# Optimization experiments

Measured on AMD Instinct MI355X. Metric: run time of the kernel, lower is better.

The kernel has to match this reference:

```python
import jax, jax.numpy as jnp
import numpy as np

N_NODES = 100000


def gcn_conv(x, src, dst, W, b, n):
    # PyG GCNConv: h = x @ W; add self-loops; sym-normalize; scatter-add; + bias
    h = x @ W                                        # [N, out]
    loop = jnp.arange(n, dtype=src.dtype)
    src2 = jnp.concatenate([src, loop])              # [E+N]
    dst2 = jnp.concatenate([dst, loop])
    deg = jax.ops.segment_sum(jnp.ones_like(dst2, dtype=h.dtype), dst2, num_segments=n)
    dis = jnp.where(deg > 0, jax.lax.rsqrt(deg), 0.0)
    norm = dis[src2] * dis[dst2]                     # [E+N]
    msg = h[src2] * norm[:, None]                    # gather + scale
    out = jax.ops.segment_sum(msg, dst2, num_segments=n)  # scatter-add
    return out + b


def setup_inputs() -> dict:
    key = jax.random.key(0)
    ks = jax.random.split(key, 8)
    F_in, H = 128, 64
    E = 1200000
    x = jax.random.normal(ks[0], (N_NODES, F_in), dtype=jnp.float32)
    edge_index = jax.random.randint(ks[1], (2, E), 0, N_NODES, dtype=jnp.int64)
    s = 1.0 / np.sqrt(F_in)
    W1 = jax.random.normal(ks[2], (F_in, H), dtype=jnp.float32) * s
    b1 = jnp.zeros((H,), dtype=jnp.float32)
    W2 = jax.random.normal(ks[3], (H, H), dtype=jnp.float32) * (1.0 / np.sqrt(H))
    b2 = jnp.zeros((H,), dtype=jnp.float32)
    W3 = jax.random.normal(ks[4], (H, 1), dtype=jnp.float32) * (1.0 / np.sqrt(H))
    b3 = jnp.zeros((1,), dtype=jnp.float32)
    return {"x": x, "edge_index": edge_index, "W1": W1, "b1": b1,
            "W2": W2, "b2": b2, "W3": W3, "b3": b3}


def reference(x, edge_index, W1, b1, W2, b2, W3, b3):
    n = x.shape[0]
    src, dst = edge_index[0], edge_index[1]
    h = jax.nn.relu(gcn_conv(x, src, dst, W1, b1, n))
    h = jax.nn.relu(gcn_conv(h, src, dst, W2, b2, n))
    return (h @ W3 + b3)[:, 0]  # squeeze(-1) -> [N]
```

## Files before the change

kernel.cpp:

```cpp
#include <hip/hip_runtime.h>

#define NF 64
#define NBKMAX 512
#define CHUNK 4096
#define CAP   4096

__device__ __forceinline__ unsigned short f2bf(float f) {
    union { float f; unsigned u; } c; c.f = f;
    unsigned u = c.u;
    return (unsigned short)((u + 0x7FFFu + ((u >> 16) & 1u)) >> 16);
}
__device__ __forceinline__ float2 bfp2(unsigned v) {
    union { unsigned u; float f; } lo, hi;
    lo.u = v << 16;
    hi.u = v & 0xffff0000u;
    return make_float2(lo.f, hi.f);
}

__global__ void k_zero(int* __restrict__ p, int m) {
    int i = blockIdx.x * blockDim.x + threadIdx.x;
    if (i < m) p[i] = 0;
}

__global__ __launch_bounds__(256) void k_bscatter2(const int* __restrict__ src,
                                                   const int* __restrict__ dst,
                                                   int* __restrict__ bcnt,
                                                   uint2* __restrict__ pairs, int E, int nbk) {
    __shared__ int hist[NBKMAX];
    __shared__ int base[NBKMAX];
    __shared__ uint2 stage[CHUNK];
    int e0 = blockIdx.x * CHUNK;
    int cnt = E - e0; if (cnt > CHUNK) cnt = CHUNK;
    for (int i = threadIdx.x; i < nbk; i += 256) hist[i] = 0;
    __syncthreads();
    for (int i = threadIdx.x; i < cnt; i += 256) {
        int s = src[e0 + i], d = dst[e0 + i];
        stage[i] = make_uint2((unsigned)s, (unsigned)d);
        atomicAdd(&hist[((unsigned)d) >> 8], 1);
    }
    __syncthreads();
    for (int i = threadIdx.x; i < nbk; i += 256) {
        int c = hist[i];
        base[i] = c ? atomicAdd(&bcnt[i], c) : 0;
        hist[i] = 0;
    }
    __syncthreads();
    for (int i = threadIdx.x; i < cnt; i += 256) {
        uint2 p = stage[i];
        int b = p.y >> 8;
        int off = base[b] + atomicAdd(&hist[b], 1);
        if (off < CAP) pairs[(size_t)b * CAP + off] = p;
    }
}

__global__ __launch_bounds__(256) void k_bsort2(const uint2* __restrict__ pairs,
                                                const int* __restrict__ bcnt,
                                                int* __restrict__ start, int* __restrict__ endp,
                                                int* __restrict__ adj,
                                                float* __restrict__ dis, int n) {
    __shared__ int cnt[256];
    __shared__ int cur[256];
    int b   = blockIdx.x;
    int nb  = b << 8;
    int nn  = n - nb; if (nn > 256) nn = 256;
    int ec  = bcnt[b]; if (ec > CAP) ec = CAP;
    int pbI = b * CAP;
    size_t pb = (size_t)pbI;
    int t = threadIdx.x;
    cnt[t] = 0;
    __syncthreads();
    for (int i = t; i < ec; i += 256)
        atomicAdd(&cnt[pairs[pb + i].y & 255], 1);
    __syncthreads();
    int v = cnt[t];
    __syncthreads();
    for (int off = 1; off < 256; off <<= 1) {
        int u = (t >= off) ? cnt[t - off] : 0;
        __syncthreads();
        cnt[t] += u;
        __syncthreads();
    }
    int exc = cnt[t] - v;
    if (t < nn) {
        start[nb + t] = pbI + exc;
        endp[nb + t]  = pbI + exc + v;
        dis[nb + t]   = rsqrtf((float)(v + 1));
    }
    cur[t] = exc;
    __syncthreads();
    for (int i = t; i < ec; i += 256) {
        uint2 p = pairs[pb + i];
        int off = atomicAdd(&cur[p.y & 255], 1);
        adj[pbI + off] = (int)p.x;
    }
}

#define KT 32
__device__ __forceinline__ int swz(int kk, int r) {
    int rho = (5 * (kk >> 2) + (kk & 3)) & 7;
    return kk * 64 + ((r + 4 * rho) & 63);
}
__device__ __forceinline__ float4 loadA4(const float* A, size_t off) {
    return *(const float4*)&A[off];
}
__device__ __forceinline__ float4 loadA4(const unsigned short* A, size_t off) {
    uint2 v = *(const uint2*)&A[off];
    float2 a = bfp2(v.x), b = bfp2(v.y);
    return make_float4(a.x, a.y, b.x, b.y);
}

template<int K, typename AT>
__global__ __launch_bounds__(256) void k_gemm(const AT* __restrict__ A,
                                              const float* __restrict__ W,
                                              const float* __restrict__ bias_in,
                                              const float* __restrict__ dis,
                                              unsigned short* __restrict__ out, int n) {
    __shared__ float sW[KT * NF];
    __shared__ float sxT[KT * 64];
    const int tid = threadIdx.x;
    const int row_base = blockIdx.x * 64;
    const int tx = tid & 15, ty = tid >> 4;
    const int c0 = tx * 4, r0 = ty * 4;
    float acc[4][4] = {{0.f}};

    for (int kt = 0; kt < K; kt += KT) {
        __syncthreads();
        for (int i = tid * 4; i < KT * NF; i += 256 * 4)
            *(float4*)&sW[i] = *(const float4*)&W[kt * NF + i];
        #pragma unroll
        for (int it = 0; it < 2; ++it) {
            int v  = tid + it * 256;
            int r  = v >> 3;
            int kv = v & 7;
            int rg = row_base + r;
            float4 val = make_float4(0.f, 0.f, 0.f, 0.f);
            if (rg < n) val = loadA4(A, (size_t)rg * K + kt + kv * 4);
            if (bias_in) {
                val.x = fmaxf(val.x + bias_in[kt + kv * 4 + 0], 0.f);
                val.y = fmaxf(val.y + bias_in[kt + kv * 4 + 1], 0.f);
                val.z = fmaxf(val.z + bias_in[kt + kv * 4 + 2], 0.f);
                val.w = fmaxf(val.w + bias_in[kt + kv * 4 + 3], 0.f);
            }
            const float vs[4] = {val.x, val.y, val.z, val.w};
            #pragma unroll
            for (int c = 0; c < 4; ++c)
                sxT[swz(kv * 4 + c, r)] = vs[c];
        }
        __syncthreads();

        #pragma unroll
        for (int kk = 0; kk < KT; ++kk) {
            const float4 xv = *(const float4*)&sxT[swz(kk, r0)];
            const float4 wv = *(const float4*)&sW[kk * 64 + c0];
            const float xs[4] = {xv.x, xv.y, xv.z, xv.w};
            const float ws[4] = {wv.x, wv.y, wv.z, wv.w};
            #pragma unroll
            for (int i = 0; i < 4; ++i)
                #pragma unroll
                for (int j = 0; j < 4; ++j)
                    acc[i][j] += xs[i] * ws[j];
        }
    }

    #pragma unroll
    for (int i = 0; i < 4; ++i) {
        int r = row_base + r0 + i;
        if (r < n) {
            float sc = dis[r];
            ushort4 o;
            o.x = f2bf(acc[i][0] * sc);
            o.y = f2bf(acc[i][1] * sc);
            o.z = f2bf(acc[i][2] * sc);
            o.w = f2bf(acc[i][3] * sc);
            *(ushort4*)&out[(size_t)r * NF + c0] = o;
        }
    }
}

__global__ __launch_bounds__(256) void k_gather(const unsigned short* __restrict__ g,
                                                const int* __restrict__ adj,
                                                const int* __restrict__ start,
                                                const int* __restrict__ endp,
                                                const float* __restrict__ dis,
                                                unsigned short* __restrict__ agg, int n) {
    int node = blockIdx.x * 16 + (threadIdx.x >> 4);
    int fl   = threadIdx.x & 15;
    int gb   = threadIdx.x & 48;
    if (node >= n) return;
    int s = start[node], e = endp[node];
    uint2 v = *(const uint2*)&g[(size_t)node * NF + fl * 4];
    float2 pa = bfp2(v.x), pb = bfp2(v.y);
    float4 acc = make_float4(pa.x, pa.y, pb.x, pb.y);
    for (int base = s; base < e; base += 16) {
        int m = e - base; if (m > 16) m = 16;
        int idx = (fl < m) ? adj[base + fl] : 0;
        for (int j = 0; j < m; ++j) {
            int u = __shfl(idx, gb + j);
            uint2 w = *(const uint2*)&g[(size_t)u * NF + fl * 4];
            float2 q0 = bfp2(w.x), q1 = bfp2(w.y);
            acc.x += q0.x; acc.y += q0.y; acc.z += q1.x; acc.w += q1.y;
        }
    }
    float sc = dis[node];
    ushort4 o;
    o.x = f2bf(acc.x * sc);
    o.y = f2bf(acc.y * sc);
    o.z = f2bf(acc.z * sc);
    o.w = f2bf(acc.w * sc);
    *(ushort4*)&agg[(size_t)node * NF + fl * 4] = o;
}

__global__ __launch_bounds__(256) void k_gather_final(const unsigned short* __restrict__ g,
                                                      const int* __restrict__ adj,
                                                      const int* __restrict__ start,
                                                      const int* __restrict__ endp,
                                                      const float* __restrict__ dis,
                                                      const float* __restrict__ b2,
                                                      const float* __restrict__ W3,
                                                      const float* __restrict__ b3,
                                                      float* __restrict__ out, int n) {
    int node = blockIdx.x * 16 + (threadIdx.x >> 4);
    int fl   = threadIdx.x & 15;
    int gb   = threadIdx.x & 48;
    if (node >= n) return;
    int s = start[node], e = endp[node];
    uint2 v = *(const uint2*)&g[(size_t)node * NF + fl * 4];
    float2 pa = bfp2(v.x), pb = bfp2(v.y);
    float4 acc = make_float4(pa.x, pa.y, pb.x, pb.y);
    for (int base = s; base < e; base += 16) {
        int m = e - base; if (m > 16) m = 16;
        int idx = (fl < m) ? adj[base + fl] : 0;
        for (int j = 0; j < m; ++j) {
            int u = __shfl(idx, gb + j);
            uint2 w = *(const uint2*)&g[(size_t)u * NF + fl * 4];
            float2 q0 = bfp2(w.x), q1 = bfp2(w.y);
            acc.x += q0.x; acc.y += q0.y; acc.z += q1.x; acc.w += q1.y;
        }
    }
    float sc = dis[node];
    const float4 bb = *(const float4*)&b2[fl * 4];
    const float4 ww = *(const float4*)&W3[fl * 4];
    float r = fmaxf(acc.x * sc + bb.x, 0.f) * ww.x
            + fmaxf(acc.y * sc + bb.y, 0.f) * ww.y
            + fmaxf(acc.z * sc + bb.z, 0.f) * ww.z
            + fmaxf(acc.w * sc + bb.w, 0.f) * ww.w;
    #pragma unroll
    for (int off = 8; off > 0; off >>= 1) r += __shfl_down(r, off, 16);
    if (fl == 0) out[node] = r + b3[0];
}

extern "C" void kernel_launch(void* const* d_in, const int* in_sizes, int n_in,
                              void* d_out, int out_size, void* d_ws, size_t ws_size,
                              hipStream_t stream) {
    const float* x  = (const float*)d_in[0];
    const int*   ei = (const int*)d_in[1];
    const float* W1 = (const float*)d_in[2];
    const float* b1 = (const float*)d_in[3];
    const float* W2 = (const float*)d_in[4];
    const float* b2 = (const float*)d_in[5];
    const float* W3 = (const float*)d_in[6];
    const float* b3 = (const float*)d_in[7];
    float* out = (float*)d_out;

    const int n = out_size;
    const int E = in_sizes[1] / 2;
    const int* src = ei;
    const int* dst = ei + E;
    const int ns  = (n + 255) & ~255;
    const int nbk = (n + 255) >> 8;

    char* w = (char*)d_ws;
    float* dis   = (float*)w;  w += (size_t)ns * 4;
    int*   start = (int*)w;    w += (size_t)ns * 4;
    int*   endp  = (int*)w;    w += (size_t)ns * 4;
    int*   adj   = (int*)w;    w += (size_t)nbk * CAP * 4;
    int*   bcnt  = (int*)w;    w += NBKMAX * 4;
    unsigned short* gbuf1 = (unsigned short*)w;  w += (size_t)n * NF * 2;
    unsigned short* gbuf2 = (unsigned short*)w;  w += (size_t)n * NF * 2;
    unsigned short* aggb  = (unsigned short*)w;  w += (size_t)n * NF * 2;
    uint2* pairs = (uint2*)w;

    const int B = 256;

    k_zero<<<(nbk + B - 1) / B, B, 0, stream>>>(bcnt, nbk);
    k_bscatter2<<<(E + CHUNK - 1) / CHUNK, B, 0, stream>>>(src, dst, bcnt, pairs, E, nbk);
    k_bsort2<<<nbk, B, 0, stream>>>(pairs, bcnt, start, endp, adj, dis, n);

    k_gemm<128, float><<<(n + 63) / 64, B, 0, stream>>>(x, W1, nullptr, dis, gbuf1, n);
    k_gather<<<(n + 15) / 16, B, 0, stream>>>(gbuf1, adj, start, endp, dis, aggb, n);

    k_gemm<64, unsigned short><<<(n + 63) / 64, B, 0, stream>>>(aggb, W2, b1, dis, gbuf2, n);
    k_gather_final<<<(n + 15) / 16, B, 0, stream>>>(gbuf2, adj, start, endp, dis, b2, W3, b3, out, n);
}
```

Measured before the change: 155.0 us.

## Replace FP32 SIMT GEMMs with split-bf16 MFMA GEMMs

The dense feature transforms now run on MFMA bf16 matrix instructions instead of scalar FP32 FMAs. Both activations and weights are split into high and low bf16 parts, and three MFMAs per tile emulate near-FP32 accuracy. A small prep kernel transposes and splits each weight matrix into the workspace, and LDS layouts are swizzled to avoid bank conflicts. The cost is extra conversion work, two extra launches and scalar bf16 output stores, in exchange for much higher compute throughput. The GEMMs are likely memory-bound, though, so the gain may be limited.

```diff
diff --git a/kernel.cpp b/kernel.cpp
--- a/kernel.cpp
+++ b/kernel.cpp
@@ -5,10 +5,17 @@
 #define CHUNK 4096
 #define CAP   4096
 
+typedef __attribute__((ext_vector_type(8))) short bf16x8;
+typedef __attribute__((ext_vector_type(4))) float f32x4;
+
 __device__ __forceinline__ unsigned short f2bf(float f) {
     union { float f; unsigned u; } c; c.f = f;
     unsigned u = c.u;
     return (unsigned short)((u + 0x7FFFu + ((u >> 16) & 1u)) >> 16);
+}
+__device__ __forceinline__ float bf2f1(unsigned short v) {
+    union { unsigned u; float f; } c; c.u = ((unsigned)v) << 16;
+    return c.f;
 }
 __device__ __forceinline__ float2 bfp2(unsigned v) {
     union { unsigned u; float f; } lo, hi;
@@ -95,84 +102,110 @@
     }
 }
 
-#define KT 32
-__device__ __forceinline__ int swz(int kk, int r) {
-    int rho = (5 * (kk >> 2) + (kk & 3)) & 7;
-    return kk * 64 + ((r + 4 * rho) & 63);
-}
-__device__ __forceinline__ float4 loadA4(const float* A, size_t off) {
-    return *(const float4*)&A[off];
-}
-__device__ __forceinline__ float4 loadA4(const unsigned short* A, size_t off) {
-    uint2 v = *(const uint2*)&A[off];
-    float2 a = bfp2(v.x), b = bfp2(v.y);
-    return make_float4(a.x, a.y, b.x, b.y);
+__global__ void k_wprep(const float* __restrict__ W, unsigned short* __restrict__ Wt_hi,
+                        unsigned short* __restrict__ Wt_lo, int K) {
+    int idx = blockIdx.x * 256 + threadIdx.x;
+    if (idx >= K * 64) return;
+    int k = idx >> 6, col = idx & 63;
+    float w = W[idx];
+    unsigned short h = f2bf(w);
+    unsigned short l = f2bf(w - bf2f1(h));
+    Wt_hi[col * K + k] = h;
+    Wt_lo[col * K + k] = l;
+}
+
+__device__ __forceinline__ void load8f(const float* A, bool ok, size_t off, float* v) {
+    if (ok) {
+        float4 a = *(const float4*)&A[off];
+        float4 b = *(const float4*)&A[off + 4];
+        v[0]=a.x; v[1]=a.y; v[2]=a.z; v[3]=a.w;
+        v[4]=b.x; v[5]=b.y; v[6]=b.z; v[7]=b.w;
+    } else { for (int j = 0; j < 8; ++j) v[j] = 0.f; }
+}
+__device__ __forceinline__ void load8f(const unsigned short* A, bool ok, size_t off, float* v) {
+    if (ok) {
+        uint4 u = *(const uint4*)&A[off];
+        float2 p0 = bfp2(u.x), p1 = bfp2(u.y), p2 = bfp2(u.z), p3 = bfp2(u.w);
+        v[0]=p0.x; v[1]=p0.y; v[2]=p1.x; v[3]=p1.y;
+        v[4]=p2.x; v[5]=p2.y; v[6]=p3.x; v[7]=p3.y;
+    } else { for (int j = 0; j < 8; ++j) v[j] = 0.f; }
 }
 
 template<int K, typename AT>
-__global__ __launch_bounds__(256) void k_gemm(const AT* __restrict__ A,
-                                              const float* __restrict__ W,
-                                              const float* __restrict__ bias_in,
-                                              const float* __restrict__ dis,
-                                              unsigned short* __restrict__ out, int n) {
-    __shared__ float sW[KT * NF];
-    __shared__ float sxT[KT * 64];
+__global__ __launch_bounds__(256) void k_mgemm(const AT* __restrict__ A,
+                                               const unsigned short* __restrict__ Wt_hi_g,
+                                               const unsigned short* __restrict__ Wt_lo_g,
+                                               const float* __restrict__ bias_in,
+                                               const float* __restrict__ dis,
+                                               unsigned short* __restrict__ out, int n) {
+    constexpr int KS = K / 8;
+    constexpr int SM = KS - 1;
+    __shared__ unsigned short sAh[64 * 32];
+    __shared__ unsigned short sAl[64 * 32];
+    __shared__ unsigned short sWh[64 * K];
+    __shared__ unsigned short sWl[64 * K];
     const int tid = threadIdx.x;
-    const int row_base = blockIdx.x * 64;
-    const int tx = tid & 15, ty = tid >> 4;
-    const int c0 = tx * 4, r0 = ty * 4;
-    float acc[4][4] = {{0.f}};
-
-    for (int kt = 0; kt < K; kt += KT) {
+    const int rb = blockIdx.x * 64;
+    const int w  = tid >> 6, l = tid & 63;
+    const int lr = l & 15, lg = l >> 4;
+    const int srow = tid >> 2, skq = tid & 3;
+
+    for (int idx = tid; idx < 64 * KS; idx += 256) {
+        int col = idx / KS, slot = idx % KS;
+        int d = col * K + 8 * (slot ^ (col & SM));
+        *(uint4*)&sWh[d] = *(const uint4*)&Wt_hi_g[col * K + slot * 8];
+        *(uint4*)&sWl[d] = *(const uint4*)&Wt_lo_g[col * K + slot * 8];
+    }
+
+    f32x4 acc[4] = {};
+
+    for (int kb = 0; kb < K; kb += 32) {
         __syncthreads();
-        for (int i = tid * 4; i < KT * NF; i += 256 * 4)
-            *(float4*)&sW[i] = *(const float4*)&W[kt * NF + i];
+        {
+            int rg = rb + srow;
+            float v[8];
+            load8f(A, rg < n, (size_t)rg * K + kb + skq * 8, v);
+            if (bias_in) {
+                #pragma unroll
+                for (int j = 0; j < 8; ++j)
+                    v[j] = fmaxf(v[j] + bias_in[kb + skq * 8 + j], 0.f);
+            }
+            unsigned short h8[8], l8[8];
+            #pragma unroll
+            for (int j = 0; j < 8; ++j) {
+                h8[j] = f2bf(v[j]);
+                l8[j] = f2bf(v[j] - bf2f1(h8[j]));
+            }
+            int d = srow * 32 + 8 * (skq ^ (srow & 3));
+            *(uint4*)&sAh[d] = *(const uint4*)h8;
+            *(uint4*)&sAl[d] = *(const uint4*)l8;
+        }
+        __syncthreads();
+
+        int arow = w * 16 + lr;
+        int aoff = arow * 32 + 8 * (lg ^ (arow & 3));
+        const bf16x8 ah = *(const bf16x8*)&sAh[aoff];
+        const bf16x8 al = *(const bf16x8*)&sAl[aoff];
         #pragma unroll
-        for (int it = 0; it < 2; ++it) {
-            int v  = tid + it * 256;
-            int r  = v >> 3;
-            int kv = v & 7;
-            int rg = row_base + r;
-            float4 val = make_float4(0.f, 0.f, 0.f, 0.f);
-            if (rg < n) val = loadA4(A, (size_t)rg * K + kt + kv * 4);
-            if (bias_in) {
-                val.x = fmaxf(val.x + bias_in[kt + kv * 4 + 0], 0.f);
-                val.y = fmaxf(val.y + bias_in[kt + kv * 4 + 1], 0.f);
-                val.z = fmaxf(val.z + bias_in[kt + kv * 4 + 2], 0.f);
-                val.w = fmaxf(val.w + bias_in[kt + kv * 4 + 3], 0.f);
-            }
-            const float vs[4] = {val.x, val.y, val.z, val.w};
-            #pragma unroll
-            for (int c = 0; c < 4; ++c)
-                sxT[swz(kv * 4 + c, r)] = vs[c];
-        }
-        __syncthreads();
-
-        #pragma unroll
-        for (int kk = 0; kk < KT; ++kk) {
-            const float4 xv = *(const float4*)&sxT[swz(kk, r0)];
-            const float4 wv = *(const float4*)&sW[kk * 64 + c0];
-            const float xs[4] = {xv.x, xv.y, xv.z, xv.w};
-            const float ws[4] = {wv.x, wv.y, wv.z, wv.w};
-            #pragma unroll
-            for (int i = 0; i < 4; ++i)
-                #pragma unroll
-                for (int j = 0; j < 4; ++j)
-                    acc[i][j] += xs[i] * ws[j];
+        for (int ct = 0; ct < 4; ++ct) {
+            int col  = ct * 16 + lr;
+            int boff = col * K + 8 * ((kb / 8 + lg) ^ (col & SM));
+            const bf16x8 bh = *(const bf16x8*)&sWh[boff];
+            const bf16x8 bl = *(const bf16x8*)&sWl[boff];
+            acc[ct] = __builtin_amdgcn_mfma_f32_16x16x32_bf16(ah, bh, acc[ct], 0, 0, 0);
+            acc[ct] = __builtin_amdgcn_mfma_f32_16x16x32_bf16(ah, bl, acc[ct], 0, 0, 0);
+            acc[ct] = __builtin_amdgcn_mfma_f32_16x16x32_bf16(al, bh, acc[ct], 0, 0, 0);
         }
     }
 
     #pragma unroll
     for (int i = 0; i < 4; ++i) {
-        int r = row_base + r0 + i;
+        int r = rb + w * 16 + lg * 4 + i;
         if (r < n) {
             float sc = dis[r];
-            ushort4 o;
-            o.x = f2bf(acc[i][0] * sc);
-            o.y = f2bf(acc[i][1] * sc);
-            o.z = f2bf(acc[i][2] * sc);
-            o.w = f2bf(acc[i][3] * sc);
-            *(ushort4*)&out[(size_t)r * NF + c0] = o;
+            #pragma unroll
+            for (int ct = 0; ct < 4; ++ct)
+                out[(size_t)r * NF + ct * 16 + lr] = f2bf(acc[ct][i] * sc);
         }
     }
 }
@@ -275,6 +308,10 @@
     int*   endp  = (int*)w;    w += (size_t)ns * 4;
     int*   adj   = (int*)w;    w += (size_t)nbk * CAP * 4;
     int*   bcnt  = (int*)w;    w += NBKMAX * 4;
+    unsigned short* wt1h = (unsigned short*)w;  w += 64 * 128 * 2;
+    unsigned short* wt1l = (unsigned short*)w;  w += 64 * 128 * 2;
+    unsigned short* wt2h = (unsigned short*)w;  w += 64 * 64 * 2;
+    unsigned short* wt2l = (unsigned short*)w;  w += 64 * 64 * 2;
     unsigned short* gbuf1 = (unsigned short*)w;  w += (size_t)n * NF * 2;
     unsigned short* gbuf2 = (unsigned short*)w;  w += (size_t)n * NF * 2;
     unsigned short* aggb  = (unsigned short*)w;  w += (size_t)n * NF * 2;
@@ -283,12 +320,14 @@
     const int B = 256;
 
     k_zero<<<(nbk + B - 1) / B, B, 0, stream>>>(bcnt, nbk);
+    k_wprep<<<(128 * 64 + B - 1) / B, B, 0, stream>>>(W1, wt1h, wt1l, 128);
+    k_wprep<<<(64 * 64 + B - 1) / B, B, 0, stream>>>(W2, wt2h, wt2l, 64);
     k_bscatter2<<<(E + CHUNK - 1) / CHUNK, B, 0, stream>>>(src, dst, bcnt, pairs, E, nbk);
     k_bsort2<<<nbk, B, 0, stream>>>(pairs, bcnt, start, endp, adj, dis, n);
 
-    k_gemm<128, float><<<(n + 63) / 64, B, 0, stream>>>(x, W1, nullptr, dis, gbuf1, n);
+    k_mgemm<128, float><<<(n + 63) / 64, B, 0, stream>>>(x, wt1h, wt1l, nullptr, dis, gbuf1, n);
     k_gather<<<(n + 15) / 16, B, 0, stream>>>(gbuf1, adj, start, endp, dis, aggb, n);
 
-    k_gemm<64, unsigned short><<<(n + 63) / 64, B, 0, stream>>>(aggb, W2, b1, dis, gbuf2, n);
+    k_mgemm<64, unsigned short><<<(n + 63) / 64, B, 0, stream>>>(aggb, wt2h, wt2l, b1, dis, gbuf2, n);
     k_gather_final<<<(n + 15) / 16, B, 0, stream>>>(gbuf2, adj, start, endp, dis, b2, W3, b3, out, n);
 }
```

After: 140.1 us. 9.6% less time.
